# Kernel tuning notes

Measured on AMD Instinct MI355X. Metric: run time of the kernel, lower is better.

## Reference

```python
import jax, jax.numpy as jnp
import numpy as np

NUM_HEADS = 8  # init num_heads


def setup_inputs() -> dict:
    key = jax.random.key(0)
    ks = jax.random.split(key, 8)
    B, N, C, G = 2, 256 * 256, 256, 512  # N hardcoded by original reshape(256*256)
    xq = jax.random.normal(ks[0], (B, N, C), jnp.float32)
    xk = jax.random.normal(ks[1], (B, N, C), jnp.float32)
    xv = jax.random.normal(ks[2], (B, N, C), jnp.float32)
    w_scale = C ** -0.5
    Wq = jax.random.normal(ks[3], (C, C), jnp.float32) * w_scale
    bq = jax.random.normal(ks[4], (C,), jnp.float32) * 0.02
    Wp = jax.random.normal(ks[5], (C, C), jnp.float32) * w_scale
    bp = jax.random.normal(ks[6], (C,), jnp.float32) * 0.02
    # Voronoi cell labels 1..G, each cell exactly N//G tokens, randomly scattered
    # over the 256x256 grid (irregular gather/scatter access, all cells < 1500 tokens).
    labels = jnp.repeat(jnp.arange(1, G + 1, dtype=jnp.int32), N // G)
    Voronoi = jnp.stack([
        jax.random.permutation(jax.random.fold_in(ks[7], b), labels) for b in range(B)
    ]).reshape(B, 256, 256)
    return {"xq": xq, "xk": xk, "xv": xv, "Wq": Wq, "bq": bq,
            "Wp": Wp, "bp": bp, "Voronoi": Voronoi, "num_groups": G}


def reference(xq, xk, xv, Wq, bq, Wp, bp, Voronoi, num_groups):
    B, N, C = xq.shape
    H = NUM_HEADS
    hd = C // H
    scale = hd ** -0.5  # qk_scale default: head_dim ** -0.5
    # NOTE: the original forward projects q, k AND v with self.q (shared weights/bias).
    # This (likely a bug upstream) is preserved faithfully here.
    q = (xq @ Wq.T + bq).reshape(B, N, H, hd)
    k = (xk @ Wq.T + bq).reshape(B, N, H, hd)
    v = (xv @ Wq.T + bq).reshape(B, N, H, hd)
    labels = Voronoi.reshape(B, N)
    order = jnp.argsort(labels, axis=1)   # [B, N] sort tokens by Voronoi cell id
    inv = jnp.argsort(order, axis=1)      # inverse permutation for scatter-back
    S = N // num_groups                   # tokens per cell (static)

    def gather(t):  # [B, N, H, hd] -> [B, G, S, H, hd] grouped by cell
        return jnp.take_along_axis(t, order[:, :, None, None], axis=1).reshape(B, num_groups, S, H, hd)

    qg = gather(q) * scale
    kg = gather(k)
    vg = gather(v)
    attn = jnp.einsum('bgshd,bgthd->bghst', qg, kg)   # per-cell scores [B,G,H,S,S]
    p = jax.nn.softmax(attn, axis=-1)                 # attn_drop=0 (eval)
    og = jnp.einsum('bghst,bgthd->bgshd', p, vg).reshape(B, N, H, hd)
    out = jnp.take_along_axis(og, inv[:, :, None, None], axis=1).reshape(B, N, C)
    return out @ Wp.T + bp                            # proj_drop=0 (eval)
```

## Files before the change

### kernel.cpp

```cpp
#include <hip/hip_runtime.h>
#include <hip/hip_bf16.h>

#define B_    2
#define NTOK  65536
#define C_    256
#define H_    8
#define HD_   32
#define G_    512
#define S_    128
#define BN    (B_*NTOK)
#define M3    (3*BN)

typedef __attribute__((ext_vector_type(8))) short short8;
typedef __attribute__((ext_vector_type(4))) float f32x4;

__device__ __forceinline__ ushort f2bf(float f) {
  __bf16 h = (__bf16)f;
  return __builtin_bit_cast(unsigned short, h);
}
__device__ __forceinline__ unsigned pk2(float lo, float hi) {
  return (unsigned)f2bf(lo) | ((unsigned)f2bf(hi) << 16);
}

__device__ __forceinline__ void gl16(const void* g, void* l) {
  __builtin_amdgcn_global_load_lds(
      (const __attribute__((address_space(1))) unsigned int*)g,
      (__attribute__((address_space(3))) unsigned int*)l, 16, 0, 0);
}

#define SW4(c, r) ((((c) ^ (r) ^ ((r) >> 2))) & 3)
#define SWK32(c, r) ((((c) ^ ((r) >> 1))) & 3)
#define VSL(c, ch) ((((c) ^ (((ch) & 7) << 1) ^ (((ch) >> 3) & 3))) & 15)

#define QSCALE 0.25506907131737264f

__global__ __launch_bounds__(256) void k_prep_group(
    const float* __restrict__ Wq, const float* __restrict__ Wp,
    ushort* __restrict__ Wq_img, ushort* __restrict__ Wp_img,
    const int* __restrict__ vor, int* __restrict__ grp,
    int* __restrict__ cnt) {
  int bid = blockIdx.x;
  if (bid < 64) {
    int gid = bid * 256 + threadIdx.x;
    int w = gid >> 13, rem = gid & 8191;
    if (w == 0) {
      int ks = rem >> 11, rem2 = rem & 2047;
      int r = rem2 >> 3, c = rem2 & 7;
      const float4* s = reinterpret_cast<const float4*>(Wq + (size_t)r * 256 + ks * 64 + c * 8);
      float4 a = s[0], b = s[1];
      uint4 o;
      o.x = pk2(a.x, a.y); o.y = pk2(a.z, a.w);
      o.z = pk2(b.x, b.y); o.w = pk2(b.z, b.w);
      *reinterpret_cast<uint4*>(Wq_img + ks * 16384 + r * 64 + ((c ^ (r & 7)) << 3)) = o;
    } else {
      int h = rem >> 10, r = (rem >> 2) & 255, c = rem & 3;
      const float4* s = reinterpret_cast<const float4*>(Wp + (size_t)r * 256 + h * 32 + c * 8);
      float4 a = s[0], b = s[1];
      uint4 o;
      o.x = pk2(a.x, a.y); o.y = pk2(a.z, a.w);
      o.z = pk2(b.x, b.y); o.w = pk2(b.z, b.w);
      *reinterpret_cast<uint4*>(Wp_img + h * 8192 + r * 32 + (SWK32(c, r) << 3)) = o;
    }
  } else {
    int idx = (bid - 64) * 256 + threadIdx.x;
    int b = idx >> 16;
    int n = idx & (NTOK - 1);
    int g = vor[idx] - 1;
    int pos = atomicAdd(&cnt[(b << 9) + g], 1);
    grp[((b << 9) + g) * S_ + pos] = n;
  }
}

__global__ __launch_bounds__(512, 4) void k_proj_qkv(
    const float* __restrict__ xq, const float* __restrict__ xk,
    const float* __restrict__ xv, const ushort* __restrict__ Wq_img,
    const float* __restrict__ bq, ushort* __restrict__ qkv) {
  __shared__ ushort As[128 * 64];
  __shared__ ushort Bs[2][256 * 64];
  int mt = blockIdx.x;
  int t = mt >> 10;
  const float* A = (t == 0) ? xq : (t == 1) ? xk : xv;
  float qsc = (t == 0) ? QSCALE : 1.0f;
  size_t abase = (size_t)(mt & 1023) * 128 * 256;
  int row0 = mt * 128;

  int tid = threadIdx.x, lane = tid & 63, wave = tid >> 6;
  int l15 = lane & 15, hi = lane >> 4;
  int wr = (wave >> 2) * 64, wc = (wave & 3) * 64;
  int sr = tid >> 2, sq = tid & 3;

  const float* aptr = A + abase + (size_t)sr * 256 + sq * 16;
  int boff = wave * 4096 + lane * 16;

  f32x4 acc[4][4] = {};
  float4 ar[2][4];
  {
    const float4* p = reinterpret_cast<const float4*>(aptr);
#pragma unroll
    for (int j = 0; j < 4; ++j) ar[0][j] = p[j];
  }
#pragma unroll
  for (int j = 0; j < 4; ++j)
    gl16((const char*)Wq_img + boff + j * 1024, (char*)Bs[0] + boff + j * 1024);

#pragma unroll
  for (int ks = 0; ks < 4; ++ks) {
    uint4 w0, w1;
    w0.x = pk2(ar[ks & 1][0].x, ar[ks & 1][0].y); w0.y = pk2(ar[ks & 1][0].z, ar[ks & 1][0].w);
    w0.z = pk2(ar[ks & 1][1].x, ar[ks & 1][1].y); w0.w = pk2(ar[ks & 1][1].z, ar[ks & 1][1].w);
    w1.x = pk2(ar[ks & 1][2].x, ar[ks & 1][2].y); w1.y = pk2(ar[ks & 1][2].z, ar[ks & 1][2].w);
    w1.z = pk2(ar[ks & 1][3].x, ar[ks & 1][3].y); w1.w = pk2(ar[ks & 1][3].z, ar[ks & 1][3].w);
    *reinterpret_cast<uint4*>(&As[sr * 64 + (((sq * 2) ^ (sr & 7)) << 3)]) = w0;
    *reinterpret_cast<uint4*>(&As[sr * 64 + (((sq * 2 + 1) ^ (sr & 7)) << 3)]) = w1;
    if (ks < 3) {
      const float4* p = reinterpret_cast<const float4*>(aptr + (ks + 1) * 64);
#pragma unroll
      for (int j = 0; j < 4; ++j) ar[(ks + 1) & 1][j] = p[j];
#pragma unroll
      for (int j = 0; j < 4; ++j)
        gl16((const char*)Wq_img + (ks + 1) * 32768 + boff + j * 1024,
             (char*)Bs[(ks + 1) & 1] + boff + j * 1024);
      asm volatile("s_waitcnt vmcnt(8)" ::: "memory");
    } else {
      asm volatile("s_waitcnt vmcnt(0)" ::: "memory");
    }
    asm volatile("s_waitcnt lgkmcnt(0)" ::: "memory");
    __builtin_amdgcn_s_barrier();
    const ushort* Bcur = Bs[ks & 1];
#pragma unroll
    for (int kk = 0; kk < 2; ++kk) {
      int ck = kk * 4 + hi;
      short8 af[4], bfr[4];
#pragma unroll
      for (int m = 0; m < 4; ++m) {
        int r = wr + m * 16 + l15;
        af[m] = *reinterpret_cast<const short8*>(&As[r * 64 + ((ck ^ (r & 7)) << 3)]);
      }
#pragma unroll
      for (int n = 0; n < 4; ++n) {
        int r = wc + n * 16 + l15;
        bfr[n] = *reinterpret_cast<const short8*>(&Bcur[r * 64 + ((ck ^ (r & 7)) << 3)]);
      }
#pragma unroll
      for (int m = 0; m < 4; ++m)
#pragma unroll
        for (int n = 0; n < 4; ++n)
          acc[m][n] = __builtin_amdgcn_mfma_f32_16x16x32_bf16(af[m], bfr[n], acc[m][n], 0, 0, 0);
    }
    asm volatile("s_waitcnt lgkmcnt(0)" ::: "memory");
    __builtin_amdgcn_s_barrier();
  }

  ushort* Ot = (ushort*)Bs;
#pragma unroll
  for (int n = 0; n < 4; ++n) {
    int col = wc + n * 16 + l15;
    float bv = bq[col];
    int c = col >> 3, ci = col & 7;
#pragma unroll
    for (int m = 0; m < 4; ++m) {
      int r0 = wr + m * 16 + hi * 4;
#pragma unroll
      for (int j = 0; j < 4; ++j) {
        int r = r0 + j;
        int slot = c ^ (((r >> 2) & 3) << 1);
        Ot[r * 256 + slot * 8 + ci] = f2bf((acc[m][n][j] + bv) * qsc);
      }
    }
  }
  __syncthreads();
  {
    size_t gbase = (size_t)row0 * 256;
#pragma unroll
    for (int s = 0; s < 8; ++s) {
      int off = s * 4096 + tid * 8;
      int r = off >> 8, cc = (off >> 3) & 31;
      int slot = cc ^ (((r >> 2) & 3) << 1);
      *reinterpret_cast<uint4*>(qkv + gbase + off) =
          *reinterpret_cast<const uint4*>(Ot + r * 256 + slot * 8);
    }
  }
}

__global__ __launch_bounds__(512) void k_attn_proj(
    const ushort* __restrict__ qkv, const int* __restrict__ grp,
    const ushort* __restrict__ Wp_img, const float* __restrict__ bp,
    float* __restrict__ out) {
  __shared__ int toks[128];
  __shared__ ushort shm[32768];
  ushort* Qs  = shm;
  ushort* Ks  = shm + 4096;
  ushort* Vt  = shm + 8192;
  ushort* Oh  = shm + 12288;
  ushort* Wp0 = shm + 16384;
  ushort* Wp1 = shm + 24576;

  int bid = blockIdx.x;
  int g = bid & (G_ - 1), b = bid >> 9;
  int tid = threadIdx.x, lane = tid & 63, wave = tid >> 6;
  int l15 = lane & 15, hi = lane >> 4;
  int strip = wave * 16;
  int mg = wave >> 1, ng = wave & 1;

  if (tid < 128) toks[tid] = grp[((b << 9) + g) * S_ + tid];
  __syncthreads();

  int wpoff = wave * 1024 + lane * 16;
  gl16((const char*)Wp_img + wpoff, (char*)Wp0 + wpoff);
  gl16((const char*)Wp_img + 8192 + wpoff, (char*)Wp0 + wpoff + 8192);

  f32x4 acc[2][8] = {};

  int r_st = tid >> 2, cp = tid & 3;
  int tok_st = toks[r_st];
  size_t rowq = (size_t)(b * NTOK + tok_st) * 256;
  int chunk_t = r_st >> 3, tl = r_st & 7;

  uint4 qa, ka, va;
  {
    size_t base = rowq + cp * 8;
    qa = *reinterpret_cast<const uint4*>(qkv + base);
    ka = *reinterpret_cast<const uint4*>(qkv + (size_t)BN * 256 + base);
    va = *reinterpret_cast<const uint4*>(qkv + (size_t)2 * BN * 256 + base);
  }

  for (int h = 0; h < 8; ++h) {
    ushort* WpCur = (h & 1) ? Wp1 : Wp0;
    ushort* WpNext = (h & 1) ? Wp0 : Wp1;
    *reinterpret_cast<uint4*>(&Qs[r_st * 32 + SW4(cp, r_st) * 8]) = qa;
    *reinterpret_cast<uint4*>(&Ks[r_st * 32 + SW4(cp, r_st) * 8]) = ka;
    {
      const ushort* pv_ = reinterpret_cast<const ushort*>(&va);
#pragma unroll
      for (int e = 0; e < 8; ++e) {
        int ch = cp * 8 + e;
        Vt[ch * 128 + (VSL(chunk_t, ch) << 3) + tl] = pv_[e];
      }
    }
    asm volatile("s_waitcnt lgkmcnt(0)" ::: "memory");
    __builtin_amdgcn_s_barrier();

    if (h < 7) {
      gl16((const char*)Wp_img + (h + 1) * 16384 + wpoff, (char*)WpNext + wpoff);
      gl16((const char*)Wp_img + (h + 1) * 16384 + 8192 + wpoff, (char*)WpNext + wpoff + 8192);
      size_t base = rowq + (h + 1) * 32 + cp * 8;
      qa = *reinterpret_cast<const uint4*>(qkv + base);
      ka = *reinterpret_cast<const uint4*>(qkv + (size_t)BN * 256 + base);
      va = *reinterpret_cast<const uint4*>(qkv + (size_t)2 * BN * 256 + base);
    }

    f32x4 sacc[8] = {};
    {
      int ra = strip + l15;
      short8 qf = *reinterpret_cast<const short8*>(&Qs[ra * 32 + SW4(hi, ra) * 8]);
      __builtin_amdgcn_s_setprio(1);
#pragma unroll
      for (int n = 0; n < 8; ++n) {
        int r = n * 16 + l15;
        short8 kf = *reinterpret_cast<const short8*>(&Ks[r * 32 + SW4(hi, r) * 8]);
        sacc[n] = __builtin_amdgcn_mfma_f32_16x16x32_bf16(kf, qf, sacc[n], 0, 0, 0);
      }
      __builtin_amdgcn_s_setprio(0);
    }

    float p[8][4];
    float sum = 0.f;
#pragma unroll
    for (int n = 0; n < 8; ++n)
#pragma unroll
      for (int j = 0; j < 4; ++j) { p[n][j] = exp2f(sacc[n][j]); sum += p[n][j]; }
    sum += __shfl_xor(sum, 16);
    sum += __shfl_xor(sum, 32);
    float inv = 1.0f / sum;

    short8 paf[4];
#pragma unroll
    for (int t = 0; t < 4; ++t) {
      unsigned e0 = pk2(p[2 * t][0], p[2 * t][1]);
      unsigned e1 = pk2(p[2 * t][2], p[2 * t][3]);
      unsigned o0 = pk2(p[2 * t + 1][0], p[2 * t + 1][1]);
      unsigned o1 = pk2(p[2 * t + 1][2], p[2 * t + 1][3]);
      unsigned pe0 = __shfl_xor(e0, 16), pe1 = __shfl_xor(e1, 16);
      unsigned po0 = __shfl_xor(o0, 16), po1 = __shfl_xor(o1, 16);
      bool up = (hi & 1);
      unsigned E0 = up ? pe0 : e0, E1 = up ? pe1 : e1;
      unsigned E2 = up ? e0 : pe0, E3 = up ? e1 : pe1;
      unsigned O0 = up ? po0 : o0, O1 = up ? po1 : o1;
      unsigned O2 = up ? o0 : po0, O3 = up ? o1 : po1;
      unsigned s0 = up ? E0 : O0, s1 = up ? E1 : O1;
      unsigned s2 = up ? E2 : O2, s3 = up ? E3 : O3;
      unsigned r0 = __shfl_xor(s0, 32), r1 = __shfl_xor(s1, 32);
      unsigned r2 = __shfl_xor(s2, 32), r3 = __shfl_xor(s3, 32);
      unsigned f0, f1, f2, f3;
      if (hi == 0)      { f0 = E0; f1 = E1; f2 = E2; f3 = E3; }
      else if (hi == 3) { f0 = O0; f1 = O1; f2 = O2; f3 = O3; }
      else              { f0 = r0; f1 = r1; f2 = r2; f3 = r3; }
      union { unsigned u[4]; short8 s; } cv;
      cv.u[0] = f0; cv.u[1] = f1; cv.u[2] = f2; cv.u[3] = f3;
      paf[t] = cv.s;
    }

    f32x4 oacc[2] = {};
    __builtin_amdgcn_s_setprio(1);
#pragma unroll
    for (int t = 0; t < 4; ++t) {
      short8 bv[2];
#pragma unroll
      for (int n2 = 0; n2 < 2; ++n2) {
        int ch = n2 * 16 + l15;
        int chunk = t * 4 + hi;
        bv[n2] = *reinterpret_cast<const short8*>(&Vt[ch * 128 + (VSL(chunk, ch) << 3)]);
      }
#pragma unroll
      for (int n2 = 0; n2 < 2; ++n2)
        oacc[n2] = __builtin_amdgcn_mfma_f32_16x16x32_bf16(paf[t], bv[n2], oacc[n2], 0, 0, 0);
    }
    __builtin_amdgcn_s_setprio(0);

    float invj[4];
#pragma unroll
    for (int jr = 0; jr < 4; ++jr) invj[jr] = __shfl(inv, hi * 4 + jr);
#pragma unroll
    for (int n2 = 0; n2 < 2; ++n2)
#pragma unroll
      for (int jr = 0; jr < 4; ++jr) {
        int row = strip + hi * 4 + jr;
        int col = n2 * 16 + l15;
        Oh[row * 32 + (SWK32(col >> 3, row) << 3) + (col & 7)] = f2bf(oacc[n2][jr] * invj[jr]);
      }
    asm volatile("s_waitcnt vmcnt(5)" ::: "memory");
    asm volatile("s_waitcnt lgkmcnt(0)" ::: "memory");
    __builtin_amdgcn_s_barrier();

    {
      short8 af[2], bf[8];
#pragma unroll
      for (int m = 0; m < 2; ++m) {
        int r = mg * 32 + m * 16 + l15;
        af[m] = *reinterpret_cast<const short8*>(&Oh[r * 32 + (SWK32(hi, r) << 3)]);
      }
#pragma unroll
      for (int n = 0; n < 8; ++n) {
        int r = ng * 128 + n * 16 + l15;
        bf[n] = *reinterpret_cast<const short8*>(&WpCur[r * 32 + (SWK32(hi, r) << 3)]);
      }
      __builtin_amdgcn_s_setprio(1);
#pragma unroll
      for (int m = 0; m < 2; ++m)
#pragma unroll
        for (int n = 0; n < 8; ++n)
          acc[m][n] = __builtin_amdgcn_mfma_f32_16x16x32_bf16(af[m], bf[n], acc[m][n], 0, 0, 0);
      __builtin_amdgcn_s_setprio(0);
    }
  }

  float* Of = (float*)shm;
#pragma unroll
  for (int q = 0; q < 4; ++q) {
    __syncthreads();
    if (mg == q) {
#pragma unroll
      for (int n = 0; n < 8; ++n) {
        int col = ng * 128 + n * 16 + l15;
        float bv = bp[col];
        int c = col >> 2, ci = col & 3;
#pragma unroll
        for (int m = 0; m < 2; ++m) {
#pragma unroll
          for (int j = 0; j < 4; ++j) {
            int lr = m * 16 + hi * 4 + j;
            int slot = c ^ (((lr >> 2) & 3) << 2);
            Of[lr * 256 + slot * 4 + ci] = acc[m][n][j] + bv;
          }
        }
      }
    }
    __syncthreads();
#pragma unroll
    for (int s = 0; s < 4; ++s) {
      int off = s * 2048 + tid * 4;
      int lr = off >> 8, cc = (off >> 2) & 63;
      int slot = cc ^ (((lr >> 2) & 3) << 2);
      int tok = toks[q * 32 + lr];
      *reinterpret_cast<float4*>(out + ((size_t)(b * NTOK + tok)) * 256 + cc * 4) =
          *reinterpret_cast<const float4*>(Of + lr * 256 + slot * 4);
    }
  }
}

extern "C" void kernel_launch(void* const* d_in, const int* in_sizes, int n_in,
                              void* d_out, int out_size, void* d_ws, size_t ws_size,
                              hipStream_t stream) {
  const float* xq = (const float*)d_in[0];
  const float* xk = (const float*)d_in[1];
  const float* xv = (const float*)d_in[2];
  const float* Wq = (const float*)d_in[3];
  const float* bq = (const float*)d_in[4];
  const float* Wp = (const float*)d_in[5];
  const float* bp = (const float*)d_in[6];
  const int*   vor = (const int*)d_in[7];

  char* ws = (char*)d_ws;
  ushort* qkv    = (ushort*)ws;
  int*    grp    = (int*)(ws + (size_t)201326592);
  int*    cnt    = (int*)(ws + (size_t)201850880);
  ushort* Wq_img = (ushort*)(ws + (size_t)201854976);
  ushort* Wp_img = (ushort*)(ws + (size_t)201986048);

  hipMemsetAsync(cnt, 0, B_ * G_ * sizeof(int), stream);
  k_prep_group<<<dim3(64 + BN / 256), dim3(256), 0, stream>>>(
      Wq, Wp, Wq_img, Wp_img, vor, grp, cnt);
  k_proj_qkv<<<dim3(M3 / 128), dim3(512), 0, stream>>>(xq, xk, xv, Wq_img, bq, qkv);
  k_attn_proj<<<dim3(B_ * G_), dim3(512), 0, stream>>>(qkv, grp, Wp_img, bp, (float*)d_out);
}
```

Baseline: 307.4 us.

## Halve QKV projection M-tile and single-buffer weight LDS to raise occupancy

The QKV projection kernel now uses 64-row output tiles instead of 128, launching twice as many blocks, and drops the double-buffered weight tile in LDS for a single buffer. Each k-step loads its weight slice and waits before computing, and launch bounds ask for 6 blocks per CU instead of 4. The aim is lower LDS and register use per block so more blocks are resident to hide memory latency on this bandwidth-bound fp32-input GEMM. The cost is that weight loads no longer overlap compute within a block, and the weight matrix is re-read by twice as many blocks.

Result: faster. 298.0 us, median of 2 (-3.1%).

```diff
diff --git a/kernel.cpp b/kernel.cpp
--- a/kernel.cpp
+++ b/kernel.cpp
@@ -71,78 +71,71 @@
   }
 }
 
-__global__ __launch_bounds__(512, 4) void k_proj_qkv(
+__global__ __launch_bounds__(512, 6) void k_proj_qkv(
     const float* __restrict__ xq, const float* __restrict__ xk,
     const float* __restrict__ xv, const ushort* __restrict__ Wq_img,
     const float* __restrict__ bq, ushort* __restrict__ qkv) {
-  __shared__ ushort As[128 * 64];
-  __shared__ ushort Bs[2][256 * 64];
+  __shared__ ushort As[64 * 64];
+  __shared__ ushort Bs[256 * 64];
   int mt = blockIdx.x;
-  int t = mt >> 10;
+  int t = mt >> 11;
   const float* A = (t == 0) ? xq : (t == 1) ? xk : xv;
   float qsc = (t == 0) ? QSCALE : 1.0f;
-  size_t abase = (size_t)(mt & 1023) * 128 * 256;
-  int row0 = mt * 128;
+  size_t abase = (size_t)(mt & 2047) * 64 * 256;
+  int row0 = mt * 64;
 
   int tid = threadIdx.x, lane = tid & 63, wave = tid >> 6;
   int l15 = lane & 15, hi = lane >> 4;
-  int wr = (wave >> 2) * 64, wc = (wave & 3) * 64;
-  int sr = tid >> 2, sq = tid & 3;
-
-  const float* aptr = A + abase + (size_t)sr * 256 + sq * 16;
+  int wr = (wave >> 2) * 32, wc = (wave & 3) * 64;
+  int sr = tid >> 3, sq8 = tid & 7;
+
+  const float* aptr = A + abase + (size_t)sr * 256 + sq8 * 8;
   int boff = wave * 4096 + lane * 16;
 
-  f32x4 acc[4][4] = {};
-  float4 ar[2][4];
+  f32x4 acc[2][4] = {};
+  float4 ar[2][2];
   {
     const float4* p = reinterpret_cast<const float4*>(aptr);
-#pragma unroll
-    for (int j = 0; j < 4; ++j) ar[0][j] = p[j];
-  }
-#pragma unroll
-  for (int j = 0; j < 4; ++j)
-    gl16((const char*)Wq_img + boff + j * 1024, (char*)Bs[0] + boff + j * 1024);
+    ar[0][0] = p[0]; ar[0][1] = p[1];
+  }
 
 #pragma unroll
   for (int ks = 0; ks < 4; ++ks) {
-    uint4 w0, w1;
-    w0.x = pk2(ar[ks & 1][0].x, ar[ks & 1][0].y); w0.y = pk2(ar[ks & 1][0].z, ar[ks & 1][0].w);
-    w0.z = pk2(ar[ks & 1][1].x, ar[ks & 1][1].y); w0.w = pk2(ar[ks & 1][1].z, ar[ks & 1][1].w);
-    w1.x = pk2(ar[ks & 1][2].x, ar[ks & 1][2].y); w1.y = pk2(ar[ks & 1][2].z, ar[ks & 1][2].w);
-    w1.z = pk2(ar[ks & 1][3].x, ar[ks & 1][3].y); w1.w = pk2(ar[ks & 1][3].z, ar[ks & 1][3].w);
-    *reinterpret_cast<uint4*>(&As[sr * 64 + (((sq * 2) ^ (sr & 7)) << 3)]) = w0;
-    *reinterpret_cast<uint4*>(&As[sr * 64 + (((sq * 2 + 1) ^ (sr & 7)) << 3)]) = w1;
+#pragma unroll
+    for (int j = 0; j < 4; ++j)
+      gl16((const char*)Wq_img + ks * 32768 + boff + j * 1024,
+           (char*)Bs + boff + j * 1024);
+    {
+      uint4 w0;
+      w0.x = pk2(ar[ks & 1][0].x, ar[ks & 1][0].y); w0.y = pk2(ar[ks & 1][0].z, ar[ks & 1][0].w);
+      w0.z = pk2(ar[ks & 1][1].x, ar[ks & 1][1].y); w0.w = pk2(ar[ks & 1][1].z, ar[ks & 1][1].w);
+      *reinterpret_cast<uint4*>(&As[sr * 64 + ((sq8 ^ (sr & 7)) << 3)]) = w0;
+    }
     if (ks < 3) {
       const float4* p = reinterpret_cast<const float4*>(aptr + (ks + 1) * 64);
-#pragma unroll
-      for (int j = 0; j < 4; ++j) ar[(ks + 1) & 1][j] = p[j];
-#pragma unroll
-      for (int j = 0; j < 4; ++j)
-        gl16((const char*)Wq_img + (ks + 1) * 32768 + boff + j * 1024,
-             (char*)Bs[(ks + 1) & 1] + boff + j * 1024);
-      asm volatile("s_waitcnt vmcnt(8)" ::: "memory");
+      ar[(ks + 1) & 1][0] = p[0]; ar[(ks + 1) & 1][1] = p[1];
+      asm volatile("s_waitcnt vmcnt(2)" ::: "memory");
     } else {
       asm volatile("s_waitcnt vmcnt(0)" ::: "memory");
     }
     asm volatile("s_waitcnt lgkmcnt(0)" ::: "memory");
     __builtin_amdgcn_s_barrier();
-    const ushort* Bcur = Bs[ks & 1];
 #pragma unroll
     for (int kk = 0; kk < 2; ++kk) {
       int ck = kk * 4 + hi;
-      short8 af[4], bfr[4];
-#pragma unroll
-      for (int m = 0; m < 4; ++m) {
+      short8 af[2], bfr[4];
+#pragma unroll
+      for (int m = 0; m < 2; ++m) {
         int r = wr + m * 16 + l15;
         af[m] = *reinterpret_cast<const short8*>(&As[r * 64 + ((ck ^ (r & 7)) << 3)]);
       }
 #pragma unroll
       for (int n = 0; n < 4; ++n) {
         int r = wc + n * 16 + l15;
-        bfr[n] = *reinterpret_cast<const short8*>(&Bcur[r * 64 + ((ck ^ (r & 7)) << 3)]);
-      }
-#pragma unroll
-      for (int m = 0; m < 4; ++m)
+        bfr[n] = *reinterpret_cast<const short8*>(&Bs[r * 64 + ((ck ^ (r & 7)) << 3)]);
+      }
+#pragma unroll
+      for (int m = 0; m < 2; ++m)
 #pragma unroll
         for (int n = 0; n < 4; ++n)
           acc[m][n] = __builtin_amdgcn_mfma_f32_16x16x32_bf16(af[m], bfr[n], acc[m][n], 0, 0, 0);
@@ -151,14 +144,14 @@
     __builtin_amdgcn_s_barrier();
   }
 
-  ushort* Ot = (ushort*)Bs;
+  ushort* Ot = Bs;
 #pragma unroll
   for (int n = 0; n < 4; ++n) {
     int col = wc + n * 16 + l15;
     float bv = bq[col];
     int c = col >> 3, ci = col & 7;
 #pragma unroll
-    for (int m = 0; m < 4; ++m) {
+    for (int m = 0; m < 2; ++m) {
       int r0 = wr + m * 16 + hi * 4;
 #pragma unroll
       for (int j = 0; j < 4; ++j) {
@@ -172,7 +165,7 @@
   {
     size_t gbase = (size_t)row0 * 256;
 #pragma unroll
-    for (int s = 0; s < 8; ++s) {
+    for (int s = 0; s < 4; ++s) {
       int off = s * 4096 + tid * 8;
       int r = off >> 8, cc = (off >> 3) & 31;
       int slot = cc ^ (((r >> 2) & 3) << 1);
@@ -410,6 +403,6 @@
   hipMemsetAsync(cnt, 0, B_ * G_ * sizeof(int), stream);
   k_prep_group<<<dim3(64 + BN / 256), dim3(256), 0, stream>>>(
       Wq, Wp, Wq_img, Wp_img, vor, grp, cnt);
-  k_proj_qkv<<<dim3(M3 / 128), dim3(512), 0, stream>>>(xq, xk, xv, Wq_img, bq, qkv);
+  k_proj_qkv<<<dim3(M3 / 64), dim3(512), 0, stream>>>(xq, xk, xv, Wq_img, bq, qkv);
   k_attn_proj<<<dim3(B_ * G_), dim3(512), 0, stream>>>(qkv, grp, Wp_img, bp, (float*)d_out);
 }
```
